# Optimization experiments

Measured on AMD Instinct MI355X. Metric: run time of the kernel, lower is better.

## Reference

```python
import jax, jax.numpy as jnp
import numpy as np
import math


def setup_inputs() -> dict:
    key = jax.random.key(0)
    k1, k2, k3, k4 = jax.random.split(key, 4)
    B, L, H, D = 2, 4096, 8, 64
    factor = 5
    U = factor * int(np.ceil(np.log(L)))  # 45 = sample_k = n_top
    return {
        "queries": jax.random.normal(k1, (B, L, H, D), dtype=jnp.float32),
        "keys": jax.random.normal(k2, (B, L, H, D), dtype=jnp.float32),
        "values": jax.random.normal(k3, (B, L, H, D), dtype=jnp.float32),
        "index_sample": jax.random.randint(k4, (L, U), 0, L),  # sampled key ids per query
    }


def reference(queries, keys, values, index_sample):
    # ProbAttention forward, mask_flag=False (non-causal ProbSparse attention).
    B, L_Q, H, D = queries.shape
    L_K = keys.shape[1]
    Q = jnp.transpose(queries, (0, 2, 1, 3))  # (B,H,L_Q,D)
    K = jnp.transpose(keys, (0, 2, 1, 3))     # (B,H,L_K,D)
    V = jnp.transpose(values, (0, 2, 1, 3))   # (B,H,L_K,D)
    n_top = index_sample.shape[1]             # U = factor*ceil(ln(L_K)) = sample_k = n_top

    # --- _prob_QK: score each query against a random subset of keys ---
    K_sample = K[:, :, index_sample, :]                     # (B,H,L_Q,sample_k,D)
    Q_K_sample = jnp.einsum('bhqd,bhqsd->bhqs', Q, K_sample)
    # sparsity measure M = max - mean (sum divided by full L_K, as in source)
    M = Q_K_sample.max(-1) - Q_K_sample.sum(-1) / L_K       # (B,H,L_Q)
    _, M_top = jax.lax.top_k(M, n_top)                      # (B,H,n_top)

    # full attention scores only for the selected top queries
    Q_reduce = jnp.take_along_axis(Q, M_top[..., None], axis=2)  # (B,H,n_top,D)
    scale = 1.0 / math.sqrt(D)
    scores = jnp.einsum('bhud,bhkd->bhuk', Q_reduce, K) * scale  # (B,H,n_top,L_K)
    attn = jax.nn.softmax(scores, axis=-1)

    # --- initial context (mask_flag=False): cumulative sum of V ---
    context = jnp.cumsum(V, axis=2)                         # (B,H,L_Q,D)

    # --- scatter attention outputs into the top-query rows ---
    update = jnp.einsum('bhuk,bhkd->bhud', attn, V)         # (B,H,n_top,D)
    bi = jnp.arange(B)[:, None, None]
    hi = jnp.arange(H)[None, :, None]
    context = context.at[bi, hi, M_top].set(update)

    return jnp.transpose(context, (0, 2, 1, 3))             # (B,L_Q,H,D)
```

## Files before the change

### kernel.cpp

```cpp
#include <hip/hip_runtime.h>
#include <math.h>

#define BB 2
#define LL 4096
#define HH 8
#define DD 64
#define UU 45
#define TILE 128
#define NTILES (LL / TILE)

#define NC 64
#define CK (LL / NC)
#define KSTR 68
#define SSTR 68

#define NB_CM (BB * HH * LL / 4)
#define NB_TS (BB * HH * NTILES)
#define NB_CU (BB * HH * NTILES)
#define NB_CO (BB * HH * UU / 4)

__device__ __forceinline__ int qkv_idx(int b, int l, int h, int d) {
    return ((b * LL + l) * HH + h) * DD + d;
}

template <int CTRL>
__device__ __forceinline__ float dpp_add(float v) {
    int x = __builtin_amdgcn_update_dpp(0, __float_as_int(v), CTRL, 0xF, 0xF,
                                        true);
    return v + __int_as_float(x);
}

__global__ __launch_bounds__(256, 2) void k_computeM_tilesum(
        const float* __restrict__ Q, const float* __restrict__ K,
        const int* __restrict__ idx, const float* __restrict__ V,
        float* __restrict__ M, float* __restrict__ tsum) {
    if (blockIdx.x >= NB_CM) {
        int blk = blockIdx.x - NB_CM;
        int tile = blk % NTILES;
        int bh = blk / NTILES;
        int h = bh % HH, b = bh / HH;
        int d = threadIdx.x & 63, g = threadIdx.x >> 6;
        const int CH = TILE / 4;
        int l0 = tile * TILE + g * CH;
        float acc = 0.f;
        for (int i = 0; i < CH; ++i) acc += V[qkv_idx(b, l0 + i, h, d)];
        __shared__ float red[4][DD];
        red[g][d] = acc;
        __syncthreads();
        if (g == 0)
            tsum[blk * DD + d] =
                red[0][d] + red[1][d] + red[2][d] + red[3][d];
        return;
    }
    int w = (blockIdx.x * blockDim.x + threadIdx.x) >> 6;
    int lane = threadIdx.x & 63;
    int q = w % LL;
    int bh = w / LL;
    int h = bh % HH, b = bh / HH;

    const float* Kbh = K + (size_t)(b * LL * HH + h) * DD;
    const size_t rowStride = (size_t)HH * DD;

    int r = lane >> 4;
    int c16 = lane & 15;

    const float4 qf = *(const float4*)(Q + qkv_idx(b, q, h, c16 * 4));
    const int* idxRow = idx + q * UU;

    int ks[12];
#pragma unroll
    for (int g = 0; g < 12; ++g) {
        int s = g * 4 + r;
        ks[g] = idxRow[s < UU ? s : 0];
    }
    float4 kk[12];
#pragma unroll
    for (int g = 0; g < 12; ++g)
        kk[g] = ((const float4*)(Kbh + (size_t)ks[g] * rowStride))[c16];

    float mval = -INFINITY, sval = 0.f;
#pragma unroll
    for (int g = 0; g < 12; ++g) {
        float part = fmaf(kk[g].x, qf.x,
                     fmaf(kk[g].y, qf.y,
                     fmaf(kk[g].z, qf.z, kk[g].w * qf.w)));
        part = dpp_add<0x128>(part);
        part = dpp_add<0x124>(part);
        part = dpp_add<0x122>(part);
        part = dpp_add<0x121>(part);
        int s = g * 4 + r;
        if (s < UU) { mval = fmaxf(mval, part); sval += part; }
    }
    mval = fmaxf(mval, __shfl_xor(mval, 16, 64));
    sval += __shfl_xor(sval, 16, 64);
    mval = fmaxf(mval, __shfl_xor(mval, 32, 64));
    sval += __shfl_xor(sval, 32, 64);
    if (lane == 0) M[bh * LL + q] = mval - sval * (1.0f / LL);
}

__global__ __launch_bounds__(1024) void k_topk(
        const float* __restrict__ M, int* __restrict__ Mtop,
        unsigned* __restrict__ selmap) {
    int bh = blockIdx.x;
    int t = threadIdx.x;
    __shared__ unsigned keys[LL];
    __shared__ unsigned hist[256];
    __shared__ unsigned scanbuf[256];
    __shared__ unsigned sPrefix, sMask, sK, sBin;
    __shared__ int outCount, eqCount;
    __shared__ int eqIdx[64];

    for (int i = t; i < LL; i += 1024) {
        unsigned u = __float_as_uint(M[bh * LL + i]);
        keys[i] = (u & 0x80000000u) ? ~u : (u | 0x80000000u);
    }
    if (selmap != nullptr && t < 128) selmap[bh * 128 + t] = 0u;
    if (t == 0) { sPrefix = 0u; sMask = 0u; sK = UU; outCount = 0; eqCount = 0; }
    __syncthreads();

    for (int pass = 0; pass < 4; ++pass) {
        int shift = 24 - pass * 8;
        if (t < 256) hist[t] = 0u;
        __syncthreads();
        unsigned prefix = sPrefix, mask = sMask;
        for (int i = t; i < LL; i += 1024) {
            unsigned k = keys[i];
            if ((k & mask) == prefix)
                atomicAdd(&hist[(k >> shift) & 0xFFu], 1u);
        }
        __syncthreads();
        if (t < 64) {
            int l = t;
            unsigned h0 = hist[4 * l + 0], h1 = hist[4 * l + 1];
            unsigned h2 = hist[4 * l + 2], h3 = hist[4 * l + 3];
            unsigned s3 = h3, s2 = h2 + s3, s1 = h1 + s2, s0 = h0 + s1;
            unsigned tot = s0, inc = tot;
#pragma unroll
            for (int off = 1; off < 64; off <<= 1) {
                unsigned x = __shfl_down(inc, off, 64);
                if (l + off < 64) inc += x;
            }
            unsigned above = inc - tot;
            scanbuf[4 * l + 0] = s0 + above;
            scanbuf[4 * l + 1] = s1 + above;
            scanbuf[4 * l + 2] = s2 + above;
            scanbuf[4 * l + 3] = s3 + above;
        }
        __syncthreads();
        if (t < 256) {
            unsigned k = sK;
            unsigned geq = scanbuf[t];
            unsigned gt = (t < 255) ? scanbuf[t + 1] : 0u;
            if (gt < k && geq >= k) sBin = (unsigned)t;
        }
        __syncthreads();
        if (t == 0) {
            unsigned b = sBin;
            unsigned gt = (b < 255u) ? scanbuf[b + 1] : 0u;
            sK -= gt;
            sPrefix |= (b << shift);
            sMask |= (0xFFu << shift);
        }
        __syncthreads();
    }
    unsigned T = sPrefix;
    int kEq = (int)sK;

    for (int i = t; i < LL; i += 1024) {
        unsigned k = keys[i];
        if (k > T) {
            int slot = atomicAdd(&outCount, 1);
            Mtop[bh * UU + slot] = i;
        } else if (k == T) {
            int e = atomicAdd(&eqCount, 1);
            if (e < 64) eqIdx[e] = i;
        }
    }
    __syncthreads();

    if (t == 0) {
        int base = outCount;
        int ec = eqCount;
        if (ec <= 64) {
            for (int s = 0; s < UU; ++s) {
                if (s >= kEq) break;
                int bi = -1, bv = LL + 2;
                for (int j = 0; j < ec; ++j) {
                    int v = eqIdx[j];
                    if (v < bv) { bv = v; bi = j; }
                }
                Mtop[bh * UU + base + s] = bv;
                eqIdx[bi] = LL + 2;
            }
        } else {
            int got = 0;
            for (int i = 0; i < LL && got < kEq; ++i)
                if (keys[i] == T) { Mtop[bh * UU + base + got] = i; ++got; }
        }
    }
    __syncthreads();
    if (selmap != nullptr && t < UU) {
        int qi = Mtop[bh * UU + t];
        atomicOr(&selmap[bh * 128 + (qi >> 5)], 1u << (qi & 31));
    }
}

__global__ __launch_bounds__(256) void k_attn_partial(
        const float* __restrict__ Q, const float* __restrict__ K,
        const float* __restrict__ V, const int* __restrict__ Mtop,
        float* __restrict__ mPart, float* __restrict__ lPart,
        float* __restrict__ Op) {
    int blk = blockIdx.x;
    int c = blk % NC;
    int bh = blk / NC;
    int h = bh % HH, b = bh / HH;
    int k0 = c * CK;
    int t = threadIdx.x;

    __shared__ float Qs[48 * KSTR];
    __shared__ float Ks[CK * KSTR];
    __shared__ float Ss[UU * SSTR];

    const size_t rowStride = (size_t)HH * DD;
    const float* Qbh = Q + (size_t)(b * LL * HH + h) * DD;
    const float* Kbh = K + (size_t)(b * LL * HH + h) * DD;
    const float* Vbh = V + (size_t)(b * LL * HH + h) * DD;

    for (int p = t; p < 48 * DD; p += 256) {
        int u = p >> 6, d = p & 63;
        float v = 0.f;
        if (u < UU) {
            int qi = Mtop[bh * UU + u];
            v = Qbh[(size_t)qi * rowStride + d] * 0.125f;
        }
        Qs[u * KSTR + d] = v;
    }
    for (int p = t; p < CK * 16; p += 256) {
        int row = p >> 4, i = p & 15;
        *(float4*)&Ks[row * KSTR + i * 4] =
            *(const float4*)&Kbh[(size_t)(k0 + row) * rowStride + i * 4];
    }
    __syncthreads();

    int kq = t & 15, uq = t >> 4;
    int u0 = uq * 3;
    float acc[3][4];
#pragma unroll
    for (int i = 0; i < 3; ++i)
#pragma unroll
        for (int j = 0; j < 4; ++j) acc[i][j] = 0.f;

#pragma unroll 4
    for (int dd = 0; dd < 16; ++dd) {
        float4 qf[3];
#pragma unroll
        for (int i = 0; i < 3; ++i)
            qf[i] = *(const float4*)&Qs[(u0 + i) * KSTR + dd * 4];
        float4 kf[4];
#pragma unroll
        for (int j = 0; j < 4; ++j)
            kf[j] = *(const float4*)&Ks[(kq + 16 * j) * KSTR + dd * 4];
#pragma unroll
        for (int i = 0; i < 3; ++i)
#pragma unroll
            for (int j = 0; j < 4; ++j) {
                acc[i][j] = fmaf(qf[i].x, kf[j].x, acc[i][j]);
                acc[i][j] = fmaf(qf[i].y, kf[j].y, acc[i][j]);
                acc[i][j] = fmaf(qf[i].z, kf[j].z, acc[i][j]);
                acc[i][j] = fmaf(qf[i].w, kf[j].w, acc[i][j]);
            }
    }
#pragma unroll
    for (int i = 0; i < 3; ++i) {
        int u = u0 + i;
        if (u < UU)
#pragma unroll
            for (int j = 0; j < 4; ++j) Ss[u * SSTR + kq + 16 * j] = acc[i][j];
    }
    __syncthreads();

    for (int p = t; p < CK * 16; p += 256) {
        int row = p >> 4, i = p & 15;
        *(float4*)&Ks[row * KSTR + i * 4] =
            *(const float4*)&Vbh[(size_t)(k0 + row) * rowStride + i * 4];
    }

    if (t < UU * 4) {
        int u = t >> 2, qq = t & 3;
        float mloc = -INFINITY;
        for (int j = 0; j < CK / 4; ++j)
            mloc = fmaxf(mloc, Ss[u * SSTR + qq + 4 * j]);
        mloc = fmaxf(mloc, __shfl_xor(mloc, 1, 64));
        mloc = fmaxf(mloc, __shfl_xor(mloc, 2, 64));
        float lloc = 0.f;
        for (int j = 0; j < CK / 4; ++j) {
            int kk = qq + 4 * j;
            float e = __expf(Ss[u * SSTR + kk] - mloc);
            Ss[u * SSTR + kk] = e;
            lloc += e;
        }
        lloc += __shfl_xor(lloc, 1, 64);
        lloc += __shfl_xor(lloc, 2, 64);
        if (qq == 0) {
            mPart[(bh * NC + c) * UU + u] = mloc;
            lPart[(bh * NC + c) * UU + u] = lloc;
        }
    }
    __syncthreads();

    int dq = t & 15;
    int d0 = dq * 4;
    if (u0 < UU) {
        float4 o[3];
#pragma unroll
        for (int i = 0; i < 3; ++i) o[i] = make_float4(0.f, 0.f, 0.f, 0.f);
#pragma unroll 4
        for (int kc = 0; kc < CK / 4; ++kc) {
            float4 vk[4];
#pragma unroll
            for (int jj = 0; jj < 4; ++jj)
                vk[jj] = *(const float4*)&Ks[(4 * kc + jj) * KSTR + d0];
#pragma unroll
            for (int i = 0; i < 3; ++i) {
                float4 pf = *(const float4*)&Ss[(u0 + i) * SSTR + 4 * kc];
                o[i].x = fmaf(pf.x, vk[0].x, o[i].x);
                o[i].y = fmaf(pf.x, vk[0].y, o[i].y);
                o[i].z = fmaf(pf.x, vk[0].z, o[i].z);
                o[i].w = fmaf(pf.x, vk[0].w, o[i].w);
                o[i].x = fmaf(pf.y, vk[1].x, o[i].x);
                o[i].y = fmaf(pf.y, vk[1].y, o[i].y);
                o[i].z = fmaf(pf.y, vk[1].z, o[i].z);
                o[i].w = fmaf(pf.y, vk[1].w, o[i].w);
                o[i].x = fmaf(pf.z, vk[2].x, o[i].x);
                o[i].y = fmaf(pf.z, vk[2].y, o[i].y);
                o[i].z = fmaf(pf.z, vk[2].z, o[i].z);
                o[i].w = fmaf(pf.z, vk[2].w, o[i].w);
                o[i].x = fmaf(pf.w, vk[3].x, o[i].x);
                o[i].y = fmaf(pf.w, vk[3].y, o[i].y);
                o[i].z = fmaf(pf.w, vk[3].z, o[i].z);
                o[i].w = fmaf(pf.w, vk[3].w, o[i].w);
            }
        }
#pragma unroll
        for (int i = 0; i < 3; ++i) {
            int u = u0 + i;
            *(float4*)&Op[((size_t)(bh * NC + c) * UU + u) * DD + d0] = o[i];
        }
    }
}

__global__ __launch_bounds__(256) void k_cumsum_combine(
        const float* __restrict__ V, const float* __restrict__ tsum,
        const unsigned* __restrict__ selmap, const int* __restrict__ Mtop,
        const float* __restrict__ mPart, const float* __restrict__ lPart,
        const float* __restrict__ Op, float* __restrict__ out) {
    int t = threadIdx.x;
    if (blockIdx.x >= NB_CU) {
        int u4 = (blockIdx.x - NB_CU) * 4 + (t >> 6);
        int u = u4 % UU;
        int bh = u4 / UU;
        int h = bh % HH, b = bh / HH;
        int d = t & 63;
        float gm = -INFINITY;
        for (int c = 0; c < NC; ++c)
            gm = fmaxf(gm, mPart[(bh * NC + c) * UU + u]);
        float denom = 0.f, acc = 0.f;
        for (int c = 0; c < NC; ++c) {
            int pi = (bh * NC + c) * UU + u;
            float w = __expf(mPart[pi] - gm);
            denom = fmaf(lPart[pi], w, denom);
            acc = fmaf(w, Op[(size_t)pi * DD + d], acc);
        }
        int qi = Mtop[bh * UU + u];
        out[qkv_idx(b, qi, h, d)] = acc / denom;
        return;
    }
    int blk = blockIdx.x;
    int tile = blk % NTILES;
    int bh = blk / NTILES;
    int h = bh % HH, b = bh / HH;
    int d = t & 63, g = t >> 6;
    const int CH = TILE / 4;
    int l0 = tile * TILE + g * CH;

    __shared__ float red[4][DD];
    __shared__ float pre2[4][DD];
    float acc = 0.f;
    for (int i = 0; i < CH; ++i) acc += V[qkv_idx(b, l0 + i, h, d)];
    red[g][d] = acc;
    float p = 0.f;
    for (int tt = g; tt < tile; tt += 4)
        p += tsum[(bh * NTILES + tt) * DD + d];
    pre2[g][d] = p;
    __syncthreads();

    float off = pre2[0][d] + pre2[1][d] + pre2[2][d] + pre2[3][d];
    for (int gg = 0; gg < g; ++gg) off += red[gg][d];

    unsigned selw = selmap[bh * 128 + (l0 >> 5)];

    float run = off;
    for (int i = 0; i < CH; ++i) {
        run += V[qkv_idx(b, l0 + i, h, d)];
        if (!((selw >> i) & 1u))
            out[qkv_idx(b, l0 + i, h, d)] = run;
    }
}

__global__ __launch_bounds__(256) void k_cumsum_fb(
        const float* __restrict__ V, const float* __restrict__ tsum,
        float* __restrict__ out) {
    int blk = blockIdx.x;
    int tile = blk % NTILES;
    int bh = blk / NTILES;
    int h = bh % HH, b = bh / HH;
    int t = threadIdx.x;
    int d = t & 63, g = t >> 6;
    const int CH = TILE / 4;
    int l0 = tile * TILE + g * CH;

    __shared__ float red[4][DD];
    __shared__ float pre2[4][DD];
    float acc = 0.f;
    for (int i = 0; i < CH; ++i) acc += V[qkv_idx(b, l0 + i, h, d)];
    red[g][d] = acc;
    float p = 0.f;
    for (int tt = g; tt < tile; tt += 4)
        p += tsum[(bh * NTILES + tt) * DD + d];
    pre2[g][d] = p;
    __syncthreads();

    float off = pre2[0][d] + pre2[1][d] + pre2[2][d] + pre2[3][d];
    for (int gg = 0; gg < g; ++gg) off += red[gg][d];

    float run = off;
    for (int i = 0; i < CH; ++i) {
        run += V[qkv_idx(b, l0 + i, h, d)];
        out[qkv_idx(b, l0 + i, h, d)] = run;
    }
}

__global__ __launch_bounds__(256) void k_attn_mono(
        const float* __restrict__ Q, const float* __restrict__ K,
        const float* __restrict__ V, const int* __restrict__ Mtop,
        float* __restrict__ out) {
    int blk = blockIdx.x;
    int u = blk % UU;
    int bh = blk / UU;
    int h = bh % HH, b = bh / HH;
    int qi = Mtop[bh * UU + u];
    int t = threadIdx.x;

    __shared__ float scores[LL];
    __shared__ float red[256];

    const float4* qp = (const float4*)(Q + qkv_idx(b, qi, h, 0));
    float4 qreg[16];
#pragma unroll
    for (int i = 0; i < 16; ++i) {
        float4 v = qp[i];
        v.x *= 0.125f; v.y *= 0.125f; v.z *= 0.125f; v.w *= 0.125f;
        qreg[i] = v;
    }

    float lmax = -INFINITY;
    for (int k = t; k < LL; k += 256) {
        const float4* kr = (const float4*)(K + qkv_idx(b, k, h, 0));
        float dot = 0.f;
#pragma unroll
        for (int i = 0; i < 16; ++i) {
            float4 kk = kr[i];
            dot = fmaf(qreg[i].x, kk.x, dot);
            dot = fmaf(qreg[i].y, kk.y, dot);
            dot = fmaf(qreg[i].z, kk.z, dot);
            dot = fmaf(qreg[i].w, kk.w, dot);
        }
        scores[k] = dot;
        lmax = fmaxf(lmax, dot);
    }
    red[t] = lmax;
    __syncthreads();
    for (int off = 128; off >= 1; off >>= 1) {
        if (t < off) red[t] = fmaxf(red[t], red[t + off]);
        __syncthreads();
    }
    float smax = red[0];
    __syncthreads();

    float lsum = 0.f;
    for (int k = t; k < LL; k += 256) {
        float e = __expf(scores[k] - smax);
        scores[k] = e;
        lsum += e;
    }
    red[t] = lsum;
    __syncthreads();
    for (int off = 128; off >= 1; off >>= 1) {
        if (t < off) red[t] += red[t + off];
        __syncthreads();
    }
    float denom = red[0];
    __syncthreads();

    int d = t & 63, g = t >> 6;
    const float4* sc4 = (const float4*)scores;
    float acc = 0.f;
    for (int kb = g; kb < LL / 4; kb += 4) {
        float4 s4 = sc4[kb];
        int kk0 = kb * 4;
        acc = fmaf(s4.x, V[qkv_idx(b, kk0 + 0, h, d)], acc);
        acc = fmaf(s4.y, V[qkv_idx(b, kk0 + 1, h, d)], acc);
        acc = fmaf(s4.z, V[qkv_idx(b, kk0 + 2, h, d)], acc);
        acc = fmaf(s4.w, V[qkv_idx(b, kk0 + 3, h, d)], acc);
    }
    red[t] = acc;
    __syncthreads();
    if (g == 0) {
        float s = red[d] + red[64 + d] + red[128 + d] + red[192 + d];
        out[qkv_idx(b, qi, h, d)] = s / denom;
    }
}

extern "C" void kernel_launch(void* const* d_in, const int* in_sizes, int n_in,
                              void* d_out, int out_size, void* d_ws, size_t ws_size,
                              hipStream_t stream) {
    const float* Q = (const float*)d_in[0];
    const float* K = (const float*)d_in[1];
    const float* V = (const float*)d_in[2];
    const int* idx = (const int*)d_in[3];
    float* out = (float*)d_out;

    float* ws = (float*)d_ws;

    const size_t M_off = 0;
    const size_t tsum_off = 65536;
    const size_t mP_off = 98304;
    const size_t lP_off = 144384;
    const size_t top_off = 190464;
    const size_t sel_off = 191488;
    const size_t Op_off = 193536;
    const size_t need = (Op_off + (size_t)BB * HH * NC * UU * DD) * 4;

    float* M = ws + M_off;
    float* tsum = ws + tsum_off;

    if (ws_size >= need) {
        float* mPart = ws + mP_off;
        float* lPart = ws + lP_off;
        int* Mtop = (int*)(ws + top_off);
        unsigned* selmap = (unsigned*)(ws + sel_off);
        float* Op = ws + Op_off;

        k_computeM_tilesum<<<NB_CM + NB_TS, 256, 0, stream>>>(Q, K, idx, V,
                                                              M, tsum);
        k_topk<<<BB * HH, 1024, 0, stream>>>(M, Mtop, selmap);
        k_attn_partial<<<BB * HH * NC, 256, 0, stream>>>(Q, K, V, Mtop,
                                                         mPart, lPart, Op);
        k_cumsum_combine<<<NB_CU + NB_CO, 256, 0, stream>>>(
            V, tsum, selmap, Mtop, mPart, lPart, Op, out);
    } else {
        int* Mtop = (int*)(ws + 65536);
        float* tsum2 = ws + 65536 + 1024;
        k_computeM_tilesum<<<NB_CM + NB_TS, 256, 0, stream>>>(Q, K, idx, V,
                                                              M, tsum2);
        k_topk<<<BB * HH, 1024, 0, stream>>>(M, Mtop, (unsigned*)nullptr);
        k_cumsum_fb<<<BB * HH * NTILES, 256, 0, stream>>>(V, tsum2, out);
        k_attn_mono<<<BB * HH * UU, 256, 0, stream>>>(Q, K, V, Mtop, out);
    }
}
```

Baseline: 185.1 us.

## Merge topk, attention, and cumsum/combine into one cooperative kernel with grid syncs

Replaces three separate launches (topk, attention partials, cumsum+combine) with a single cooperative kernel of 768 blocks that uses grid-wide syncs between phases, and falls back to the old launches if the cooperative launch fails. The intent is to remove kernel launch gaps and inter-kernel drain. In exchange, topk now runs with only 16 blocks of 256 threads while the other blocks wait at the grid barrier. Occupancy is constrained by the shared-memory union and the launch bounds.

```diff
diff --git a/kernel.cpp b/kernel.cpp
--- a/kernel.cpp
+++ b/kernel.cpp
@@ -1,5 +1,8 @@
 #include <hip/hip_runtime.h>
+#include <hip/hip_cooperative_groups.h>
 #include <math.h>
+
+namespace cg = cooperative_groups;
 
 #define BB 2
 #define LL 4096
@@ -14,10 +17,11 @@
 #define KSTR 68
 #define SSTR 68
 
-#define NB_CM (BB * HH * LL / 4)
+#define NB_CMU (BB * HH * LL / 4)
 #define NB_TS (BB * HH * NTILES)
 #define NB_CU (BB * HH * NTILES)
 #define NB_CO (BB * HH * UU / 4)
+#define GRIDB 768
 
 __device__ __forceinline__ int qkv_idx(int b, int l, int h, int d) {
     return ((b * LL + l) * HH + h) * DD + d;
@@ -30,30 +34,28 @@
     return v + __int_as_float(x);
 }
 
-__global__ __launch_bounds__(256, 2) void k_computeM_tilesum(
-        const float* __restrict__ Q, const float* __restrict__ K,
-        const int* __restrict__ idx, const float* __restrict__ V,
-        float* __restrict__ M, float* __restrict__ tsum) {
-    if (blockIdx.x >= NB_CM) {
-        int blk = blockIdx.x - NB_CM;
-        int tile = blk % NTILES;
-        int bh = blk / NTILES;
-        int h = bh % HH, b = bh / HH;
-        int d = threadIdx.x & 63, g = threadIdx.x >> 6;
-        const int CH = TILE / 4;
-        int l0 = tile * TILE + g * CH;
-        float acc = 0.f;
-        for (int i = 0; i < CH; ++i) acc += V[qkv_idx(b, l0 + i, h, d)];
-        __shared__ float red[4][DD];
-        red[g][d] = acc;
-        __syncthreads();
-        if (g == 0)
-            tsum[blk * DD + d] =
-                red[0][d] + red[1][d] + red[2][d] + red[3][d];
-        return;
-    }
-    int w = (blockIdx.x * blockDim.x + threadIdx.x) >> 6;
-    int lane = threadIdx.x & 63;
+struct SmemTopk {
+    unsigned keys[LL];
+    unsigned hist[256];
+    unsigned scanbuf[256];
+    unsigned sPrefix, sMask, sK, sBin;
+    int outCount, eqCount;
+    int eqIdx[64];
+};
+struct SmemAttn {
+    float Qs[48 * KSTR];
+    float Ks[CK * KSTR];
+    float Ss[UU * SSTR];
+};
+struct SmemSum {
+    float red[4][DD];
+    float pre2[4][DD];
+};
+
+__device__ __forceinline__ void computeM_unit(
+        int w, int lane, const float* __restrict__ Q,
+        const float* __restrict__ K, const int* __restrict__ idx,
+        float* __restrict__ M) {
     int q = w % LL;
     int bh = w / LL;
     int h = bh % HH, b = bh / HH;
@@ -98,41 +100,53 @@
     if (lane == 0) M[bh * LL + q] = mval - sval * (1.0f / LL);
 }
 
-__global__ __launch_bounds__(1024) void k_topk(
-        const float* __restrict__ M, int* __restrict__ Mtop,
-        unsigned* __restrict__ selmap) {
-    int bh = blockIdx.x;
-    int t = threadIdx.x;
-    __shared__ unsigned keys[LL];
-    __shared__ unsigned hist[256];
-    __shared__ unsigned scanbuf[256];
-    __shared__ unsigned sPrefix, sMask, sK, sBin;
-    __shared__ int outCount, eqCount;
-    __shared__ int eqIdx[64];
-
-    for (int i = t; i < LL; i += 1024) {
+__device__ __forceinline__ void tilesum_unit(
+        int blk, int t, const float* __restrict__ V, float* __restrict__ tsum,
+        float (*red)[DD]) {
+    int tile = blk % NTILES;
+    int bh = blk / NTILES;
+    int h = bh % HH, b = bh / HH;
+    int d = t & 63, g = t >> 6;
+    const int CH = TILE / 4;
+    int l0 = tile * TILE + g * CH;
+    float acc = 0.f;
+    for (int i = 0; i < CH; ++i) acc += V[qkv_idx(b, l0 + i, h, d)];
+    red[g][d] = acc;
+    __syncthreads();
+    if (g == 0)
+        tsum[blk * DD + d] = red[0][d] + red[1][d] + red[2][d] + red[3][d];
+}
+
+template <int NT>
+__device__ void topk_unit(int bh, int t, const float* __restrict__ M,
+                          int* __restrict__ Mtop,
+                          unsigned* __restrict__ selmap, SmemTopk* s) {
+    for (int i = t; i < LL; i += NT) {
         unsigned u = __float_as_uint(M[bh * LL + i]);
-        keys[i] = (u & 0x80000000u) ? ~u : (u | 0x80000000u);
+        s->keys[i] = (u & 0x80000000u) ? ~u : (u | 0x80000000u);
     }
     if (selmap != nullptr && t < 128) selmap[bh * 128 + t] = 0u;
-    if (t == 0) { sPrefix = 0u; sMask = 0u; sK = UU; outCount = 0; eqCount = 0; }
+    if (t == 0) {
+        s->sPrefix = 0u; s->sMask = 0u; s->sK = UU;
+        s->outCount = 0; s->eqCount = 0;
+    }
     __syncthreads();
 
     for (int pass = 0; pass < 4; ++pass) {
         int shift = 24 - pass * 8;
-        if (t < 256) hist[t] = 0u;
-        __syncthreads();
-        unsigned prefix = sPrefix, mask = sMask;
-        for (int i = t; i < LL; i += 1024) {
-            unsigned k = keys[i];
+        if (t < 256) s->hist[t] = 0u;
+        __syncthreads();
+        unsigned prefix = s->sPrefix, mask = s->sMask;
+        for (int i = t; i < LL; i += NT) {
+            unsigned k = s->keys[i];
             if ((k & mask) == prefix)
-                atomicAdd(&hist[(k >> shift) & 0xFFu], 1u);
+                atomicAdd(&s->hist[(k >> shift) & 0xFFu], 1u);
         }
         __syncthreads();
         if (t < 64) {
             int l = t;
-            unsigned h0 = hist[4 * l + 0], h1 = hist[4 * l + 1];
-            unsigned h2 = hist[4 * l + 2], h3 = hist[4 * l + 3];
+            unsigned h0 = s->hist[4 * l + 0], h1 = s->hist[4 * l + 1];
+            unsigned h2 = s->hist[4 * l + 2], h3 = s->hist[4 * l + 3];
             unsigned s3 = h3, s2 = h2 + s3, s1 = h1 + s2, s0 = h0 + s1;
             unsigned tot = s0, inc = tot;
 #pragma unroll
@@ -141,61 +155,61 @@
                 if (l + off < 64) inc += x;
             }
             unsigned above = inc - tot;
-            scanbuf[4 * l + 0] = s0 + above;
-            scanbuf[4 * l + 1] = s1 + above;
-            scanbuf[4 * l + 2] = s2 + above;
-            scanbuf[4 * l + 3] = s3 + above;
+            s->scanbuf[4 * l + 0] = s0 + above;
+            s->scanbuf[4 * l + 1] = s1 + above;
+            s->scanbuf[4 * l + 2] = s2 + above;
+            s->scanbuf[4 * l + 3] = s3 + above;
         }
         __syncthreads();
         if (t < 256) {
-            unsigned k = sK;
-            unsigned geq = scanbuf[t];
-            unsigned gt = (t < 255) ? scanbuf[t + 1] : 0u;
-            if (gt < k && geq >= k) sBin = (unsigned)t;
+            unsigned k = s->sK;
+            unsigned geq = s->scanbuf[t];
+            unsigned gt = (t < 255) ? s->scanbuf[t + 1] : 0u;
+            if (gt < k && geq >= k) s->sBin = (unsigned)t;
         }
         __syncthreads();
         if (t == 0) {
-            unsigned b = sBin;
-            unsigned gt = (b < 255u) ? scanbuf[b + 1] : 0u;
-            sK -= gt;
-            sPrefix |= (b << shift);
-            sMask |= (0xFFu << shift);
-        }
-        __syncthreads();
-    }
-    unsigned T = sPrefix;
-    int kEq = (int)sK;
-
-    for (int i = t; i < LL; i += 1024) {
-        unsigned k = keys[i];
+            unsigned b = s->sBin;
+            unsigned gt = (b < 255u) ? s->scanbuf[b + 1] : 0u;
+            s->sK -= gt;
+            s->sPrefix |= (b << shift);
+            s->sMask |= (0xFFu << shift);
+        }
+        __syncthreads();
+    }
+    unsigned T = s->sPrefix;
+    int kEq = (int)s->sK;
+
+    for (int i = t; i < LL; i += NT) {
+        unsigned k = s->keys[i];
         if (k > T) {
-            int slot = atomicAdd(&outCount, 1);
+            int slot = atomicAdd(&s->outCount, 1);
             Mtop[bh * UU + slot] = i;
         } else if (k == T) {
-            int e = atomicAdd(&eqCount, 1);
-            if (e < 64) eqIdx[e] = i;
+            int e = atomicAdd(&s->eqCount, 1);
+            if (e < 64) s->eqIdx[e] = i;
         }
     }
     __syncthreads();
 
     if (t == 0) {
-        int base = outCount;
-        int ec = eqCount;
+        int base = s->outCount;
+        int ec = s->eqCount;
         if (ec <= 64) {
-            for (int s = 0; s < UU; ++s) {
-                if (s >= kEq) break;
+            for (int ss = 0; ss < UU; ++ss) {
+                if (ss >= kEq) break;
                 int bi = -1, bv = LL + 2;
                 for (int j = 0; j < ec; ++j) {
-                    int v = eqIdx[j];
+                    int v = s->eqIdx[j];
                     if (v < bv) { bv = v; bi = j; }
                 }
-                Mtop[bh * UU + base + s] = bv;
-                eqIdx[bi] = LL + 2;
+                Mtop[bh * UU + base + ss] = bv;
+                s->eqIdx[bi] = LL + 2;
             }
         } else {
             int got = 0;
             for (int i = 0; i < LL && got < kEq; ++i)
-                if (keys[i] == T) { Mtop[bh * UU + base + got] = i; ++got; }
+                if (s->keys[i] == T) { Mtop[bh * UU + base + got] = i; ++got; }
         }
     }
     __syncthreads();
@@ -205,21 +219,13 @@
     }
 }
 
-__global__ __launch_bounds__(256) void k_attn_partial(
+__device__ void attn_unit(int bh, int c, int t,
         const float* __restrict__ Q, const float* __restrict__ K,
         const float* __restrict__ V, const int* __restrict__ Mtop,
         float* __restrict__ mPart, float* __restrict__ lPart,
-        float* __restrict__ Op) {
-    int blk = blockIdx.x;
-    int c = blk % NC;
-    int bh = blk / NC;
+        float* __restrict__ Op, SmemAttn* s) {
     int h = bh % HH, b = bh / HH;
     int k0 = c * CK;
-    int t = threadIdx.x;
-
-    __shared__ float Qs[48 * KSTR];
-    __shared__ float Ks[CK * KSTR];
-    __shared__ float Ss[UU * SSTR];
 
     const size_t rowStride = (size_t)HH * DD;
     const float* Qbh = Q + (size_t)(b * LL * HH + h) * DD;
@@ -233,11 +239,11 @@
             int qi = Mtop[bh * UU + u];
             v = Qbh[(size_t)qi * rowStride + d] * 0.125f;
         }
-        Qs[u * KSTR + d] = v;
+        s->Qs[u * KSTR + d] = v;
     }
     for (int p = t; p < CK * 16; p += 256) {
         int row = p >> 4, i = p & 15;
-        *(float4*)&Ks[row * KSTR + i * 4] =
+        *(float4*)&s->Ks[row * KSTR + i * 4] =
             *(const float4*)&Kbh[(size_t)(k0 + row) * rowStride + i * 4];
     }
     __syncthreads();
@@ -255,11 +261,11 @@
         float4 qf[3];
 #pragma unroll
         for (int i = 0; i < 3; ++i)
-            qf[i] = *(const float4*)&Qs[(u0 + i) * KSTR + dd * 4];
+            qf[i] = *(const float4*)&s->Qs[(u0 + i) * KSTR + dd * 4];
         float4 kf[4];
 #pragma unroll
         for (int j = 0; j < 4; ++j)
-            kf[j] = *(const float4*)&Ks[(kq + 16 * j) * KSTR + dd * 4];
+            kf[j] = *(const float4*)&s->Ks[(kq + 16 * j) * KSTR + dd * 4];
 #pragma unroll
         for (int i = 0; i < 3; ++i)
 #pragma unroll
@@ -275,13 +281,14 @@
         int u = u0 + i;
         if (u < UU)
 #pragma unroll
-            for (int j = 0; j < 4; ++j) Ss[u * SSTR + kq + 16 * j] = acc[i][j];
+            for (int j = 0; j < 4; ++j)
+                s->Ss[u * SSTR + kq + 16 * j] = acc[i][j];
     }
     __syncthreads();
 
     for (int p = t; p < CK * 16; p += 256) {
         int row = p >> 4, i = p & 15;
-        *(float4*)&Ks[row * KSTR + i * 4] =
+        *(float4*)&s->Ks[row * KSTR + i * 4] =
             *(const float4*)&Vbh[(size_t)(k0 + row) * rowStride + i * 4];
     }
 
@@ -289,14 +296,14 @@
         int u = t >> 2, qq = t & 3;
         float mloc = -INFINITY;
         for (int j = 0; j < CK / 4; ++j)
-            mloc = fmaxf(mloc, Ss[u * SSTR + qq + 4 * j]);
+            mloc = fmaxf(mloc, s->Ss[u * SSTR + qq + 4 * j]);
         mloc = fmaxf(mloc, __shfl_xor(mloc, 1, 64));
         mloc = fmaxf(mloc, __shfl_xor(mloc, 2, 64));
         float lloc = 0.f;
         for (int j = 0; j < CK / 4; ++j) {
             int kk = qq + 4 * j;
-            float e = __expf(Ss[u * SSTR + kk] - mloc);
-            Ss[u * SSTR + kk] = e;
+            float e = __expf(s->Ss[u * SSTR + kk] - mloc);
+            s->Ss[u * SSTR + kk] = e;
             lloc += e;
         }
         lloc += __shfl_xor(lloc, 1, 64);
@@ -319,10 +326,10 @@
             float4 vk[4];
 #pragma unroll
             for (int jj = 0; jj < 4; ++jj)
-                vk[jj] = *(const float4*)&Ks[(4 * kc + jj) * KSTR + d0];
+                vk[jj] = *(const float4*)&s->Ks[(4 * kc + jj) * KSTR + d0];
 #pragma unroll
             for (int i = 0; i < 3; ++i) {
-                float4 pf = *(const float4*)&Ss[(u0 + i) * SSTR + 4 * kc];
+                float4 pf = *(const float4*)&s->Ss[(u0 + i) * SSTR + 4 * kc];
                 o[i].x = fmaf(pf.x, vk[0].x, o[i].x);
                 o[i].y = fmaf(pf.x, vk[0].y, o[i].y);
                 o[i].z = fmaf(pf.x, vk[0].z, o[i].z);
@@ -349,33 +356,9 @@
     }
 }
 
-__global__ __launch_bounds__(256) void k_cumsum_combine(
-        const float* __restrict__ V, const float* __restrict__ tsum,
-        const unsigned* __restrict__ selmap, const int* __restrict__ Mtop,
-        const float* __restrict__ mPart, const float* __restrict__ lPart,
-        const float* __restrict__ Op, float* __restrict__ out) {
-    int t = threadIdx.x;
-    if (blockIdx.x >= NB_CU) {
-        int u4 = (blockIdx.x - NB_CU) * 4 + (t >> 6);
-        int u = u4 % UU;
-        int bh = u4 / UU;
-        int h = bh % HH, b = bh / HH;
-        int d = t & 63;
-        float gm = -INFINITY;
-        for (int c = 0; c < NC; ++c)
-            gm = fmaxf(gm, mPart[(bh * NC + c) * UU + u]);
-        float denom = 0.f, acc = 0.f;
-        for (int c = 0; c < NC; ++c) {
-            int pi = (bh * NC + c) * UU + u;
-            float w = __expf(mPart[pi] - gm);
-            denom = fmaf(lPart[pi], w, denom);
-            acc = fmaf(w, Op[(size_t)pi * DD + d], acc);
-        }
-        int qi = Mtop[bh * UU + u];
-        out[qkv_idx(b, qi, h, d)] = acc / denom;
-        return;
-    }
-    int blk = blockIdx.x;
+__device__ void cumsum_unit(int blk, int t, const float* __restrict__ V,
+        const float* __restrict__ tsum, const unsigned* __restrict__ selmap,
+        float* __restrict__ out, SmemSum* s) {
     int tile = blk % NTILES;
     int bh = blk / NTILES;
     int h = bh % HH, b = bh / HH;
@@ -383,21 +366,19 @@
     const int CH = TILE / 4;
     int l0 = tile * TILE + g * CH;
 
-    __shared__ float red[4][DD];
-    __shared__ float pre2[4][DD];
     float acc = 0.f;
     for (int i = 0; i < CH; ++i) acc += V[qkv_idx(b, l0 + i, h, d)];
-    red[g][d] = acc;
+    s->red[g][d] = acc;
     float p = 0.f;
     for (int tt = g; tt < tile; tt += 4)
         p += tsum[(bh * NTILES + tt) * DD + d];
-    pre2[g][d] = p;
-    __syncthreads();
-
-    float off = pre2[0][d] + pre2[1][d] + pre2[2][d] + pre2[3][d];
-    for (int gg = 0; gg < g; ++gg) off += red[gg][d];
-
-    unsigned selw = selmap[bh * 128 + (l0 >> 5)];
+    s->pre2[g][d] = p;
+    __syncthreads();
+
+    float off = s->pre2[0][d] + s->pre2[1][d] + s->pre2[2][d] + s->pre2[3][d];
+    for (int gg = 0; gg < g; ++gg) off += s->red[gg][d];
+
+    unsigned selw = (selmap != nullptr) ? selmap[bh * 128 + (l0 >> 5)] : 0u;
 
     float run = off;
     for (int i = 0; i < CH; ++i) {
@@ -407,37 +388,110 @@
     }
 }
 
+__device__ __forceinline__ void combine_unit(
+        int u4, int d, const int* __restrict__ Mtop,
+        const float* __restrict__ mPart, const float* __restrict__ lPart,
+        const float* __restrict__ Op, float* __restrict__ out) {
+    int u = u4 % UU;
+    int bh = u4 / UU;
+    int h = bh % HH, b = bh / HH;
+    float gm = -INFINITY;
+    for (int c = 0; c < NC; ++c)
+        gm = fmaxf(gm, mPart[(bh * NC + c) * UU + u]);
+    float denom = 0.f, acc = 0.f;
+    for (int c = 0; c < NC; ++c) {
+        int pi = (bh * NC + c) * UU + u;
+        float w = __expf(mPart[pi] - gm);
+        denom = fmaf(lPart[pi], w, denom);
+        acc = fmaf(w, Op[(size_t)pi * DD + d], acc);
+    }
+    int qi = Mtop[bh * UU + u];
+    out[qkv_idx(b, qi, h, d)] = acc / denom;
+}
+
+__global__ __launch_bounds__(256, 2) void k_computeM_tilesum(
+        const float* __restrict__ Q, const float* __restrict__ K,
+        const int* __restrict__ idx, const float* __restrict__ V,
+        float* __restrict__ M, float* __restrict__ tsum) {
+    __shared__ float red[4][DD];
+    if (blockIdx.x >= NB_CMU) {
+        tilesum_unit(blockIdx.x - NB_CMU, threadIdx.x, V, tsum, red);
+        return;
+    }
+    computeM_unit(blockIdx.x * 4 + (threadIdx.x >> 6), threadIdx.x & 63,
+                  Q, K, idx, M);
+}
+
+__global__ __launch_bounds__(256, 3) void k_coop(
+        const float* __restrict__ Q, const float* __restrict__ K,
+        const float* __restrict__ V, const float* __restrict__ M,
+        const float* __restrict__ tsum, float* __restrict__ mPart,
+        float* __restrict__ lPart, int* __restrict__ Mtop,
+        unsigned* __restrict__ selmap, float* __restrict__ Op,
+        float* __restrict__ out) {
+    cg::grid_group grid = cg::this_grid();
+    __shared__ __align__(16) char smem[sizeof(SmemAttn)];
+    int t = threadIdx.x;
+    int bid = blockIdx.x;
+
+    if (bid < BB * HH)
+        topk_unit<256>(bid, t, M, Mtop, selmap, (SmemTopk*)smem);
+    grid.sync();
+
+    for (int u = bid; u < BB * HH * NC; u += GRIDB) {
+        attn_unit(u / NC, u % NC, t, Q, K, V, Mtop, mPart, lPart, Op,
+                  (SmemAttn*)smem);
+        __syncthreads();
+    }
+    grid.sync();
+
+    for (int u = bid; u < NB_CU + NB_CO; u += GRIDB) {
+        if (u < NB_CU)
+            cumsum_unit(u, t, V, tsum, selmap, out, (SmemSum*)smem);
+        else
+            combine_unit((u - NB_CU) * 4 + (t >> 6), t & 63, Mtop, mPart,
+                         lPart, Op, out);
+    }
+}
+
+__global__ __launch_bounds__(1024) void k_topk(
+        const float* __restrict__ M, int* __restrict__ Mtop,
+        unsigned* __restrict__ selmap) {
+    __shared__ SmemTopk s;
+    topk_unit<1024>(blockIdx.x, threadIdx.x, M, Mtop, selmap, &s);
+}
+
+__global__ __launch_bounds__(256) void k_attn_partial(
+        const float* __restrict__ Q, const float* __restrict__ K,
+        const float* __restrict__ V, const int* __restrict__ Mtop,
+        float* __restrict__ mPart, float* __restrict__ lPart,
+        float* __restrict__ Op) {
+    __shared__ SmemAttn s;
+    attn_unit(blockIdx.x / NC, blockIdx.x % NC, threadIdx.x, Q, K, V, Mtop,
+              mPart, lPart, Op, &s);
+}
+
+__global__ __launch_bounds__(256) void k_cumsum_combine(
+        const float* __restrict__ V, const float* __restrict__ tsum,
+        const unsigned* __restrict__ selmap, const int* __restrict__ Mtop,
+        const float* __restrict__ mPart, const float* __restrict__ lPart,
+        const float* __restrict__ Op, float* __restrict__ out) {
+    __shared__ SmemSum s;
+    int t = threadIdx.x;
+    if (blockIdx.x >= NB_CU) {
+        combine_unit((blockIdx.x - NB_CU) * 4 + (t >> 6), t & 63, Mtop,
+                     mPart, lPart, Op, out);
+        return;
+    }
+    cumsum_unit(blockIdx.x, t, V, tsum, selmap, out, &s);
+}
+
 __global__ __launch_bounds__(256) void k_cumsum_fb(
         const float* __restrict__ V, const float* __restrict__ tsum,
         float* __restrict__ out) {
-    int blk = blockIdx.x;
-    int tile = blk % NTILES;
-    int bh = blk / NTILES;
-    int h = bh % HH, b = bh / HH;
-    int t = threadIdx.x;
-    int d = t & 63, g = t >> 6;
-    const int CH = TILE / 4;
-    int l0 = tile * TILE + g * CH;
-
-    __shared__ float red[4][DD];
-    __shared__ float pre2[4][DD];
-    float acc = 0.f;
-    for (int i = 0; i < CH; ++i) acc += V[qkv_idx(b, l0 + i, h, d)];
-    red[g][d] = acc;
-    float p = 0.f;
-    for (int tt = g; tt < tile; tt += 4)
-        p += tsum[(bh * NTILES + tt) * DD + d];
-    pre2[g][d] = p;
-    __syncthreads();
-
-    float off = pre2[0][d] + pre2[1][d] + pre2[2][d] + pre2[3][d];
-    for (int gg = 0; gg < g; ++gg) off += red[gg][d];
-
-    float run = off;
-    for (int i = 0; i < CH; ++i) {
-        run += V[qkv_idx(b, l0 + i, h, d)];
-        out[qkv_idx(b, l0 + i, h, d)] = run;
-    }
+    __shared__ SmemSum s;
+    cumsum_unit(blockIdx.x, threadIdx.x, V, tsum, (const unsigned*)nullptr,
+                out, &s);
 }
 
 __global__ __launch_bounds__(256) void k_attn_mono(
@@ -551,18 +605,27 @@
         unsigned* selmap = (unsigned*)(ws + sel_off);
         float* Op = ws + Op_off;
 
-        k_computeM_tilesum<<<NB_CM + NB_TS, 256, 0, stream>>>(Q, K, idx, V,
-                                                              M, tsum);
-        k_topk<<<BB * HH, 1024, 0, stream>>>(M, Mtop, selmap);
-        k_attn_partial<<<BB * HH * NC, 256, 0, stream>>>(Q, K, V, Mtop,
-                                                         mPart, lPart, Op);
-        k_cumsum_combine<<<NB_CU + NB_CO, 256, 0, stream>>>(
-            V, tsum, selmap, Mtop, mPart, lPart, Op, out);
+        k_computeM_tilesum<<<NB_CMU + NB_TS, 256, 0, stream>>>(Q, K, idx, V,
+                                                               M, tsum);
+
+        void* kargs[] = {(void*)&Q, (void*)&K, (void*)&V, (void*)&M,
+                         (void*)&tsum, (void*)&mPart, (void*)&lPart,
+                         (void*)&Mtop, (void*)&selmap, (void*)&Op,
+                         (void*)&out};
+        hipError_t ce = hipLaunchCooperativeKernel(
+            (void*)k_coop, dim3(GRIDB), dim3(256), kargs, 0, stream);
+        if (ce != hipSuccess) {
+            k_topk<<<BB * HH, 1024, 0, stream>>>(M, Mtop, selmap);
+            k_attn_partial<<<BB * HH * NC, 256, 0, stream>>>(Q, K, V, Mtop,
+                                                             mPart, lPart, Op);
+            k_cumsum_combine<<<NB_CU + NB_CO, 256, 0, stream>>>(
+                V, tsum, selmap, Mtop, mPart, lPart, Op, out);
+        }
     } else {
         int* Mtop = (int*)(ws + 65536);
         float* tsum2 = ws + 65536 + 1024;
-        k_computeM_tilesum<<<NB_CM + NB_TS, 256, 0, stream>>>(Q, K, idx, V,
-                                                              M, tsum2);
+        k_computeM_tilesum<<<NB_CMU + NB_TS, 256, 0, stream>>>(Q, K, idx, V,
+                                                               M, tsum2);
         k_topk<<<BB * HH, 1024, 0, stream>>>(M, Mtop, (unsigned*)nullptr);
         k_cumsum_fb<<<BB * HH * NTILES, 256, 0, stream>>>(V, tsum2, out);
         k_attn_mono<<<BB * HH * UU, 256, 0, stream>>>(Q, K, V, Mtop, out);
```

New measurement: 321.6 us. 1.74x slower.
